# Kernel optimization log

Measured on AMD Instinct MI355X. Metric: run time of the kernel, lower is better.

The kernel has to match this reference:

```python
import jax, jax.numpy as jnp
import numpy as np

N = 100000      # num nodes
E = 1600000     # num edges
NFEAT = 512
NHID = 256
NCLASS = 32
K = 10
ALPHA = 0.1


def setup_inputs() -> dict:
    key = jax.random.key(0)
    ks = jax.random.split(key, 6)
    x = jax.random.normal(ks[0], (N, NFEAT), dtype=jnp.float32)
    edge_index = jax.random.randint(ks[1], (2, E), 0, N, dtype=jnp.int32)
    edge_attr = jax.random.uniform(ks[2], (E,), dtype=jnp.float32)
    # Linear params (Kaiming-ish scale)
    W_start = jax.random.normal(ks[3], (NFEAT, NHID), dtype=jnp.float32) * np.float32(1.0 / np.sqrt(NFEAT))
    b_start = jnp.zeros((NHID,), jnp.float32)
    W_end = jax.random.normal(ks[4], (NHID, NCLASS), dtype=jnp.float32) * np.float32(1.0 / np.sqrt(NHID))
    b_end = jnp.zeros((NCLASS,), jnp.float32)
    # GPR 'PPR' init coefficients: temp[k] = alpha*(1-alpha)^k, temp[K] = (1-alpha)^K
    temp = (ALPHA * (1.0 - ALPHA) ** np.arange(K + 1)).astype(np.float32)
    temp[-1] = np.float32((1.0 - ALPHA) ** K)
    temp = jnp.asarray(temp)
    return {"x": x, "edge_attr": edge_attr, "W_start": W_start, "b_start": b_start,
            "W_end": W_end, "b_end": b_end, "temp": temp, "edge_index": edge_index}


def gcn_norm(edge_index, edge_weight, num_nodes):
    # add self loops with weight 1 (PyG default fill_value=1)
    loop = jnp.arange(num_nodes, dtype=edge_index.dtype)
    ei = jnp.concatenate([edge_index, jnp.stack([loop, loop])], axis=1)   # [2, E+N]
    ew = jnp.concatenate([edge_weight, jnp.ones((num_nodes,), edge_weight.dtype)])
    row, col = ei[0], ei[1]
    deg = jax.ops.segment_sum(ew, col, num_segments=num_nodes)            # [N]
    dis = jnp.where(deg > 0, jax.lax.rsqrt(jnp.where(deg > 0, deg, 1.0)), 0.0)
    norm = dis[row] * ew * dis[col]                                       # [E+N]
    return ei, norm


def reference(x, edge_attr, W_start, b_start, W_end, b_end, temp, edge_index):
    # MLP front-end (eval mode: dropout is identity)
    h = jax.nn.relu(x @ W_start + b_start)        # [N, NHID]
    h = jax.nn.relu(h @ W_end + b_end)            # [N, NCLASS]
    ei, norm = gcn_norm(edge_index, edge_attr, N)
    row, col = ei[0], ei[1]
    hidden = h * temp[0]
    xk = h
    for k in range(K):
        # SpMM: gather messages norm * x[row], scatter-add at col
        xk = jax.ops.segment_sum(norm[:, None] * xk[row], col, num_segments=N)
        hidden = hidden + temp[k + 1] * xk
    return hidden
```

## Files before the change

kernel.cpp:

```cpp
#include <hip/hip_runtime.h>

typedef __attribute__((ext_vector_type(8))) short short8;
typedef __attribute__((ext_vector_type(4))) float f32x4;
typedef unsigned long long u64;

constexpr int NN = 100000;
constexpr int EE = 1600000;
constexpr int NF = 512;
constexpr int NH = 256;
constexpr int NC = 32;
constexpr int KP = 10;
constexpr int PKN = EE + 8 * NN;

__device__ __forceinline__ unsigned short f2bf(float f) {
  unsigned int u = __float_as_uint(f);
  u += 0x7FFFu + ((u >> 16) & 1u);
  return (unsigned short)(u >> 16);
}
__device__ __forceinline__ float bf2f(unsigned short s) {
  return __uint_as_float(((unsigned int)s) << 16);
}
__device__ __forceinline__ int padc(int c) { return (c + 7) & ~7; }

__device__ __forceinline__ short8 cvt8(float4 a0, float4 a1) {
  union { unsigned int u[4]; short8 s; } r;
  asm("v_cvt_pk_bf16_f32 %0, %1, %2" : "=v"(r.u[0]) : "v"(a0.x), "v"(a0.y));
  asm("v_cvt_pk_bf16_f32 %0, %1, %2" : "=v"(r.u[1]) : "v"(a0.z), "v"(a0.w));
  asm("v_cvt_pk_bf16_f32 %0, %1, %2" : "=v"(r.u[2]) : "v"(a1.x), "v"(a1.y));
  asm("v_cvt_pk_bf16_f32 %0, %1, %2" : "=v"(r.u[3]) : "v"(a1.z), "v"(a1.w));
  return r.s;
}

__device__ __forceinline__ void block_sync_lds() {
  asm volatile("s_waitcnt lgkmcnt(0)" ::: "memory");
  __builtin_amdgcn_s_barrier();
}

__global__ void convwb_kernel(const float* __restrict__ Ws, const float* __restrict__ We,
                              unsigned short* __restrict__ Wt, unsigned short* __restrict__ Web) {
  if (blockIdx.x < 32) {
    __shared__ float tile[64][65];
    const int k0 = (blockIdx.x >> 2) * 64;
    const int c0 = (blockIdx.x & 3) * 64;
    const int t = threadIdx.x;
    const int g = t >> 6, l = t & 63;
#pragma unroll
    for (int j = 0; j < 16; j++) {
      const int row = g * 16 + j;
      tile[row][l] = Ws[(size_t)(k0 + row) * NH + c0 + l];
    }
    __syncthreads();
    const int col = t >> 2, ks = (t & 3) * 16;
    union { unsigned short us[16]; short8 s8[2]; } st;
#pragma unroll
    for (int i = 0; i < 16; i++) st.us[i] = f2bf(tile[ks + i][col]);
    unsigned short* dst = Wt + (size_t)(c0 + col) * NF + k0 + ks;
    *reinterpret_cast<short8*>(dst) = st.s8[0];
    *reinterpret_cast<short8*>(dst + 8) = st.s8[1];
  } else {
    const int t = threadIdx.x;
    const int col = t & 31, kb = (t >> 5) * 32;
#pragma unroll
    for (int i = 0; i < 32; i++)
      Web[(size_t)col * 256 + kb + i] = f2bf(We[(size_t)(kb + i) * NC + col]);
  }
}

__global__ __launch_bounds__(256, 3) void gemm1_kernel(
    const float* __restrict__ X, const unsigned short* __restrict__ Wt,
    const float* __restrict__ bias, const unsigned short* __restrict__ Web,
    const float* __restrict__ be, const float* __restrict__ temp,
    unsigned short* __restrict__ x0b, float* __restrict__ out) {
  constexpr int PAD = 36;
  __shared__ __align__(16) unsigned short Asm[2][64 * PAD];
  __shared__ __align__(16) unsigned short Bsm[2][256 * PAD];
  const int tid = threadIdx.x;
  const int lane = tid & 63;
  const int w = tid >> 6;
  const int l15 = lane & 15, kq = lane >> 4;
  const int m0 = blockIdx.x * 64;

  const int arl = tid >> 2, aq = tid & 3;
  int ar = m0 + arl; if (ar >= NN) ar = NN - 1;
  const float* aptr = X + (size_t)ar * NF + aq * 8;
  const int awr = arl * PAD + aq * 8;
  const unsigned short* bptr = Wt + (size_t)tid * NF;
  const int bwr = tid * PAD;

  f32x4 acc[4][4];
#pragma unroll
  for (int m = 0; m < 4; m++)
#pragma unroll
    for (int n = 0; n < 4; n++) acc[m][n] = (f32x4)0.0f;

  float4 ra[3][2]; short8 rb[3][4];

#define LOADR(ks, j) do { \
    ra[j][0] = *reinterpret_cast<const float4*>(aptr + (ks) * 32); \
    ra[j][1] = *reinterpret_cast<const float4*>(aptr + (ks) * 32 + 4); \
    rb[j][0] = *reinterpret_cast<const short8*>(bptr + (ks) * 32); \
    rb[j][1] = *reinterpret_cast<const short8*>(bptr + (ks) * 32 + 8); \
    rb[j][2] = *reinterpret_cast<const short8*>(bptr + (ks) * 32 + 16); \
    rb[j][3] = *reinterpret_cast<const short8*>(bptr + (ks) * 32 + 24); \
  } while (0)

#define STAGE(b, j) do { \
    *reinterpret_cast<short8*>(&Asm[b][awr]) = cvt8(ra[j][0], ra[j][1]); \
    *reinterpret_cast<short8*>(&Bsm[b][bwr]) = rb[j][0]; \
    *reinterpret_cast<short8*>(&Bsm[b][bwr + 8]) = rb[j][1]; \
    *reinterpret_cast<short8*>(&Bsm[b][bwr + 16]) = rb[j][2]; \
    *reinterpret_cast<short8*>(&Bsm[b][bwr + 24]) = rb[j][3]; \
  } while (0)

#define COMPUTE(b) do { \
    short8 af[4], bfr[4]; \
    _Pragma("unroll") \
    for (int mi = 0; mi < 4; mi++) \
      af[mi] = *reinterpret_cast<const short8*>(&Asm[b][(mi * 16 + l15) * PAD + kq * 8]); \
    _Pragma("unroll") \
    for (int ni = 0; ni < 4; ni++) \
      bfr[ni] = *reinterpret_cast<const short8*>(&Bsm[b][(w * 64 + ni * 16 + l15) * PAD + kq * 8]); \
    _Pragma("unroll") \
    for (int mi = 0; mi < 4; mi++) \
      _Pragma("unroll") \
      for (int ni = 0; ni < 4; ni++) \
        acc[mi][ni] = __builtin_amdgcn_mfma_f32_16x16x32_bf16(af[mi], bfr[ni], acc[mi][ni], 0, 0, 0); \
  } while (0)

  LOADR(0, 0);
  LOADR(1, 1);
  LOADR(2, 2);
  STAGE(0, 0);
  block_sync_lds();

#pragma unroll
  for (int p = 0; p < 16; p++) {
    if (p + 3 < 16) LOADR(p + 3, (p + 3) % 3);
    COMPUTE(p & 1);
    if (p + 1 < 16) STAGE((p + 1) & 1, (p + 1) % 3);
    block_sync_lds();
  }
#undef LOADR
#undef STAGE
#undef COMPUTE

  unsigned short* Ht = (unsigned short*)Bsm;
  f32x4 acc2[2];
  acc2[0] = (f32x4)0.0f; acc2[1] = (f32x4)0.0f;
  const unsigned short* wrow = Web + (size_t)l15 * 256 + kq * 8;
#pragma unroll
  for (int p2 = 0; p2 < 2; p2++) {
    block_sync_lds();
    if ((w >> 1) == p2) {
#pragma unroll
      for (int ni = 0; ni < 4; ni++) {
        const int colg = w * 64 + ni * 16 + l15;
        const float bsv = bias[colg];
        const int cl = colg - p2 * 128;
#pragma unroll
        for (int mi = 0; mi < 4; mi++)
#pragma unroll
          for (int i = 0; i < 4; i++) {
            const int row = mi * 16 + kq * 4 + i;
            const float v = acc[mi][ni][i] + bsv;
            Ht[row * 136 + cl] = f2bf(v > 0.f ? v : 0.f);
          }
      }
    }
    block_sync_lds();
    const unsigned short* hr = Ht + (size_t)(w * 16 + l15) * 136 + kq * 8;
#pragma unroll
    for (int ks = 0; ks < 4; ks++) {
      short8 a  = *reinterpret_cast<const short8*>(hr + ks * 32);
      short8 b0 = *reinterpret_cast<const short8*>(wrow + p2 * 128 + ks * 32);
      short8 b1 = *reinterpret_cast<const short8*>(wrow + 16 * 256 + p2 * 128 + ks * 32);
      acc2[0] = __builtin_amdgcn_mfma_f32_16x16x32_bf16(a, b0, acc2[0], 0, 0, 0);
      acc2[1] = __builtin_amdgcn_mfma_f32_16x16x32_bf16(a, b1, acc2[1], 0, 0, 0);
    }
  }
  const float t0 = temp[0];
#pragma unroll
  for (int nt = 0; nt < 2; nt++) {
    const int col = nt * 16 + l15;
    const float bv = be[col];
#pragma unroll
    for (int i = 0; i < 4; i++) {
      const int row = m0 + w * 16 + kq * 4 + i;
      if (row < NN) {
        float v = acc2[nt][i] + bv;
        v = v > 0.f ? v : 0.f;
        x0b[(size_t)row * NC + col] = f2bf(v);
        out[(size_t)row * NC + col] = t0 * v;
      }
    }
  }
}

__global__ void node_init_kernel(u64* dc, u64* pk) {
  int i = blockIdx.x * 256 + threadIdx.x;
  if (i < NN) dc[i] = (1ULL << 44) | (1ULL << 32);
  for (int j = i; j < PKN; j += 391 * 256) pk[j] = 0;
}

__global__ void edge_deg_kernel(const int* __restrict__ ei, const float* __restrict__ ew,
                                u64* dc) {
  int e = blockIdx.x * 256 + threadIdx.x;
  if (e < EE) {
    int col = ei[EE + e];
    u64 v = (1ULL << 44) | (u64)((double)ew[e] * 4294967296.0);
    atomicAdd(&dc[col], v);
  }
}

__global__ void dis_kernel(const u64* __restrict__ dc, float* __restrict__ dis,
                           int* __restrict__ cnt) {
  int i = blockIdx.x * 256 + threadIdx.x;
  if (i < NN) {
    u64 v = dc[i];
    cnt[i] = (int)(v >> 44);
    float deg = (float)((double)(v & 0xFFFFFFFFFFFULL) * (1.0 / 4294967296.0));
    dis[i] = rsqrtf(deg);
  }
}

__global__ void scan1_kernel(const int* __restrict__ cnt, int* bsum) {
  __shared__ int ws[4];
  const int tid = threadIdx.x;
  int base = blockIdx.x * 1024 + tid * 4;
  int s = 0;
#pragma unroll
  for (int j = 0; j < 4; j++) { int i = base + j; if (i < NN) s += padc(cnt[i]); }
  for (int off = 32; off > 0; off >>= 1) s += __shfl_down(s, off);
  if ((tid & 63) == 0) ws[tid >> 6] = s;
  __syncthreads();
  if (tid == 0) bsum[blockIdx.x] = ws[0] + ws[1] + ws[2] + ws[3];
}

__global__ void scan3_kernel(const int* __restrict__ cnt, const int* __restrict__ bsum,
                             int* offs, int* cursor) {
  __shared__ int wsum[4];
  __shared__ int bofs_s;
  const int tid = threadIdx.x;
  const int lane = tid & 63, wv = tid >> 6;
  if (tid == 0) {
    int run = 0;
    for (int i = 0; i < (int)blockIdx.x; i++) run += bsum[i];
    bofs_s = run;
    if (blockIdx.x == 0) {
      int tot = 0;
      for (int i = 0; i < 98; i++) tot += bsum[i];
      offs[NN] = tot;
    }
  }
  int base = blockIdx.x * 1024 + tid * 4;
  int v[4]; int s = 0;
#pragma unroll
  for (int j = 0; j < 4; j++) { int i = base + j; v[j] = (i < NN) ? padc(cnt[i]) : 0; s += v[j]; }
  int incl = s;
  for (int off = 1; off < 64; off <<= 1) {
    int t = __shfl_up(incl, off);
    if (lane >= off) incl += t;
  }
  if (lane == 63) wsum[wv] = incl;
  __syncthreads();
  int woff = bofs_s;
  for (int w = 0; w < wv; w++) woff += wsum[w];
  int excl = woff + incl - s;
#pragma unroll
  for (int j = 0; j < 4; j++) {
    int i = base + j;
    if (i < NN) { offs[i] = excl; cursor[i] = excl; }
    excl += v[j];
  }
}

__global__ void fill_kernel(const int* __restrict__ ei, const float* __restrict__ ew,
                            const float* __restrict__ dis, int* cursor,
                            u64* __restrict__ pk) {
  int t = blockIdx.x * 256 + threadIdx.x;
  if (t < EE) {
    int r = ei[t], c = ei[EE + t];
    int slot = atomicAdd(&cursor[c], 1);
    unsigned int wb = __float_as_uint(dis[r] * ew[t] * dis[c]);
    pk[slot] = (u64)(unsigned int)r | ((u64)wb << 32);
  } else if (t < EE + NN) {
    int i = t - EE;
    int slot = atomicAdd(&cursor[i], 1);
    float d = dis[i];
    unsigned int wb = __float_as_uint(d * d);
    pk[slot] = (u64)(unsigned int)i | ((u64)wb << 32);
  }
}

__global__ __launch_bounds__(256) void spmm_kernel(
    const int* __restrict__ offs, const u64* __restrict__ pk,
    const unsigned short* __restrict__ xin, unsigned short* __restrict__ xout) {
  const int tid = threadIdx.x;
  const int node = blockIdx.x * 32 + (tid >> 3);
  const int fq = (tid & 7) * 4;
  const int s = offs[node], e = offs[node + 1];
  float a0 = 0.f, a1 = 0.f, a2 = 0.f, a3 = 0.f;
  for (int j = s; j < e; j += 8) {
    ulonglong2 p01 = *reinterpret_cast<const ulonglong2*>(pk + j);
    ulonglong2 p23 = *reinterpret_cast<const ulonglong2*>(pk + j + 2);
    ulonglong2 p45 = *reinterpret_cast<const ulonglong2*>(pk + j + 4);
    ulonglong2 p67 = *reinterpret_cast<const ulonglong2*>(pk + j + 6);
    const u64 p[8] = {p01.x, p01.y, p23.x, p23.y, p45.x, p45.y, p67.x, p67.y};
    u64 q[8];
#pragma unroll
    for (int i = 0; i < 8; i++)
      q[i] = *reinterpret_cast<const u64*>(xin + (size_t)(unsigned int)p[i] * NC + fq);
#pragma unroll
    for (int i = 0; i < 8; i++) {
      const float w = __uint_as_float((unsigned int)(p[i] >> 32));
      a0 += w * bf2f((unsigned short)(q[i]));
      a1 += w * bf2f((unsigned short)(q[i] >> 16));
      a2 += w * bf2f((unsigned short)(q[i] >> 32));
      a3 += w * bf2f((unsigned short)(q[i] >> 48));
    }
  }
  unsigned int lo, hi;
  asm("v_cvt_pk_bf16_f32 %0, %1, %2" : "=v"(lo) : "v"(a0), "v"(a1));
  asm("v_cvt_pk_bf16_f32 %0, %1, %2" : "=v"(hi) : "v"(a2), "v"(a3));
  *reinterpret_cast<u64*>(xout + (size_t)node * NC + fq) =
      (u64)lo | ((u64)hi << 32);
}

__global__ __launch_bounds__(256) void spmm_wsum_kernel(
    const int* __restrict__ offs, const u64* __restrict__ pk,
    const unsigned short* __restrict__ xin,
    const unsigned short* __restrict__ SL,
    float* __restrict__ out, const float* __restrict__ temp) {
  const int tid = threadIdx.x;
  const int node = blockIdx.x * 32 + (tid >> 3);
  const int fq = (tid & 7) * 4;
  const int s = offs[node], e = offs[node + 1];
  float a0 = 0.f, a1 = 0.f, a2 = 0.f, a3 = 0.f;
  for (int j = s; j < e; j += 8) {
    ulonglong2 p01 = *reinterpret_cast<const ulonglong2*>(pk + j);
    ulonglong2 p23 = *reinterpret_cast<const ulonglong2*>(pk + j + 2);
    ulonglong2 p45 = *reinterpret_cast<const ulonglong2*>(pk + j + 4);
    ulonglong2 p67 = *reinterpret_cast<const ulonglong2*>(pk + j + 6);
    const u64 p[8] = {p01.x, p01.y, p23.x, p23.y, p45.x, p45.y, p67.x, p67.y};
    u64 q[8];
#pragma unroll
    for (int i = 0; i < 8; i++)
      q[i] = *reinterpret_cast<const u64*>(xin + (size_t)(unsigned int)p[i] * NC + fq);
#pragma unroll
    for (int i = 0; i < 8; i++) {
      const float w = __uint_as_float((unsigned int)(p[i] >> 32));
      a0 += w * bf2f((unsigned short)(q[i]));
      a1 += w * bf2f((unsigned short)(q[i] >> 16));
      a2 += w * bf2f((unsigned short)(q[i] >> 32));
      a3 += w * bf2f((unsigned short)(q[i] >> 48));
    }
  }
  const size_t ob = (size_t)node * NC + fq;
  float4 o = *reinterpret_cast<const float4*>(out + ob);
  const float t10 = temp[10];
  float r0 = o.x + t10 * a0, r1 = o.y + t10 * a1;
  float r2 = o.z + t10 * a2, r3 = o.w + t10 * a3;
#pragma unroll
  for (int k = 0; k < 8; k++) {
    const float tk = temp[k + 1];
    u64 q = *reinterpret_cast<const u64*>(SL + (size_t)k * NN * NC + ob);
    r0 += tk * bf2f((unsigned short)(q));
    r1 += tk * bf2f((unsigned short)(q >> 16));
    r2 += tk * bf2f((unsigned short)(q >> 32));
    r3 += tk * bf2f((unsigned short)(q >> 48));
  }
  {
    const float tk = temp[9];
    u64 q = *reinterpret_cast<const u64*>(xin + ob);
    r0 += tk * bf2f((unsigned short)(q));
    r1 += tk * bf2f((unsigned short)(q >> 16));
    r2 += tk * bf2f((unsigned short)(q >> 32));
    r3 += tk * bf2f((unsigned short)(q >> 48));
  }
  *reinterpret_cast<float4*>(out + ob) = make_float4(r0, r1, r2, r3);
}

extern "C" void kernel_launch(void* const* d_in, const int* in_sizes, int n_in,
                              void* d_out, int out_size, void* d_ws, size_t ws_size,
                              hipStream_t stream) {
  const float* X    = (const float*)d_in[0];
  const float* EA   = (const float*)d_in[1];
  const float* Ws   = (const float*)d_in[2];
  const float* bs   = (const float*)d_in[3];
  const float* We   = (const float*)d_in[4];
  const float* be   = (const float*)d_in[5];
  const float* temp = (const float*)d_in[6];
  const int*   ei   = (const int*)d_in[7];
  float* out = (float*)d_out;

  size_t off = 0;
  auto alloc = [&](size_t n) { void* p = (char*)d_ws + off; off += (n + 255) & ~(size_t)255; return p; };
  unsigned short* Wt  = (unsigned short*)alloc((size_t)NF * NH * 2);
  unsigned short* Web = (unsigned short*)alloc((size_t)NH * NC * 2);
  unsigned short* SL  = (unsigned short*)alloc((size_t)NN * NH * 2);
  unsigned short* x0b = (unsigned short*)alloc((size_t)NN * NC * 2);
  unsigned short* xk8 = (unsigned short*)alloc((size_t)NN * NC * 2);
  u64*   dc   = (u64*)alloc((size_t)NN * 8);
  float* dis  = (float*)alloc((size_t)NN * 4);
  int*   cnt  = (int*)alloc((size_t)NN * 4);
  int*   offs = (int*)alloc((size_t)(NN + 1) * 4);
  int*   cursor = (int*)alloc((size_t)NN * 4);
  int*   bsum = (int*)alloc(98 * 4);
  u64*   pk   = (u64*)alloc((size_t)PKN * 8);

  convwb_kernel<<<33, 256, 0, stream>>>(Ws, We, Wt, Web);
  gemm1_kernel<<<1563, 256, 0, stream>>>(X, Wt, bs, Web, be, temp, x0b, out);

  node_init_kernel<<<391, 256, 0, stream>>>(dc, pk);
  edge_deg_kernel<<<6250, 256, 0, stream>>>(ei, EA, dc);
  dis_kernel<<<391, 256, 0, stream>>>(dc, dis, cnt);
  scan1_kernel<<<98, 256, 0, stream>>>(cnt, bsum);
  scan3_kernel<<<98, 256, 0, stream>>>(cnt, bsum, offs, cursor);
  fill_kernel<<<6641, 256, 0, stream>>>(ei, EA, dis, cursor, pk);

  auto slice = [&](int k) -> unsigned short* {
    return (k < 8) ? SL + (size_t)k * NN * NC : xk8;
  };
  const unsigned short* xin = x0b;
  for (int k = 0; k < KP - 1; k++) {
    spmm_kernel<<<3125, 256, 0, stream>>>(offs, pk, xin, slice(k));
    xin = slice(k);
  }
  spmm_wsum_kernel<<<3125, 256, 0, stream>>>(offs, pk, xk8, SL, out, temp);
}
```

Before: 534.6 us.

## Merge preprocessing launches and co-schedule degree atomics with the GEMM

Folds weight conversion and node/pk initialisation into one prep kernel. Appends the edge-degree atomic blocks to the GEMM launch so they run concurrently with GEMM tiles. Fuses the dis computation into the first scan pass. This removes several launches and intermediate passes over the node arrays, and lets the memory-bound atomics overlap compute-heavy GEMM work. The risk is that the extra blocks in the GEMM launch compete for occupancy, since they use the same launch bounds and LDS allocation.

Result: faster. 504.3 us (-5.7%).

```diff
diff --git a/kernel.cpp b/kernel.cpp
--- a/kernel.cpp
+++ b/kernel.cpp
@@ -11,6 +11,7 @@
 constexpr int NC = 32;
 constexpr int KP = 10;
 constexpr int PKN = EE + 8 * NN;
+constexpr int GB = 1563;
 
 __device__ __forceinline__ unsigned short f2bf(float f) {
   unsigned int u = __float_as_uint(f);
@@ -36,8 +37,9 @@
   __builtin_amdgcn_s_barrier();
 }
 
-__global__ void convwb_kernel(const float* __restrict__ Ws, const float* __restrict__ We,
-                              unsigned short* __restrict__ Wt, unsigned short* __restrict__ Web) {
+__global__ void prep_kernel(const float* __restrict__ Ws, const float* __restrict__ We,
+                            unsigned short* __restrict__ Wt, unsigned short* __restrict__ Web,
+                            u64* __restrict__ dc, u64* __restrict__ pk) {
   if (blockIdx.x < 32) {
     __shared__ float tile[64][65];
     const int k0 = (blockIdx.x >> 2) * 64;
@@ -57,24 +59,40 @@
     unsigned short* dst = Wt + (size_t)(c0 + col) * NF + k0 + ks;
     *reinterpret_cast<short8*>(dst) = st.s8[0];
     *reinterpret_cast<short8*>(dst + 8) = st.s8[1];
-  } else {
+  } else if (blockIdx.x == 32) {
     const int t = threadIdx.x;
     const int col = t & 31, kb = (t >> 5) * 32;
 #pragma unroll
     for (int i = 0; i < 32; i++)
       Web[(size_t)col * 256 + kb + i] = f2bf(We[(size_t)(kb + i) * NC + col]);
-  }
-}
-
-__global__ __launch_bounds__(256, 3) void gemm1_kernel(
+  } else {
+    const int i = (blockIdx.x - 33) * 256 + threadIdx.x;
+    if (i < NN) dc[i] = (1ULL << 44) | (1ULL << 32);
+    for (int j = i; j < PKN; j += 391 * 256) pk[j] = 0;
+  }
+}
+
+__global__ __launch_bounds__(256, 3) void gemm_deg_kernel(
     const float* __restrict__ X, const unsigned short* __restrict__ Wt,
     const float* __restrict__ bias, const unsigned short* __restrict__ Web,
     const float* __restrict__ be, const float* __restrict__ temp,
-    unsigned short* __restrict__ x0b, float* __restrict__ out) {
+    unsigned short* __restrict__ x0b, float* __restrict__ out,
+    const int* __restrict__ ei, const float* __restrict__ ew, u64* dc) {
   constexpr int PAD = 36;
   __shared__ __align__(16) unsigned short Asm[2][64 * PAD];
   __shared__ __align__(16) unsigned short Bsm[2][256 * PAD];
   const int tid = threadIdx.x;
+
+  if (blockIdx.x >= GB) {
+    const int e = (blockIdx.x - GB) * 256 + tid;
+    if (e < EE) {
+      const int col = ei[EE + e];
+      u64 v = (1ULL << 44) | (u64)((double)ew[e] * 4294967296.0);
+      atomicAdd(&dc[col], v);
+    }
+    return;
+  }
+
   const int lane = tid & 63;
   const int w = tid >> 6;
   const int l15 = lane & 15, kq = lane >> 4;
@@ -196,40 +214,24 @@
   }
 }
 
-__global__ void node_init_kernel(u64* dc, u64* pk) {
-  int i = blockIdx.x * 256 + threadIdx.x;
-  if (i < NN) dc[i] = (1ULL << 44) | (1ULL << 32);
-  for (int j = i; j < PKN; j += 391 * 256) pk[j] = 0;
-}
-
-__global__ void edge_deg_kernel(const int* __restrict__ ei, const float* __restrict__ ew,
-                                u64* dc) {
-  int e = blockIdx.x * 256 + threadIdx.x;
-  if (e < EE) {
-    int col = ei[EE + e];
-    u64 v = (1ULL << 44) | (u64)((double)ew[e] * 4294967296.0);
-    atomicAdd(&dc[col], v);
-  }
-}
-
-__global__ void dis_kernel(const u64* __restrict__ dc, float* __restrict__ dis,
-                           int* __restrict__ cnt) {
-  int i = blockIdx.x * 256 + threadIdx.x;
-  if (i < NN) {
-    u64 v = dc[i];
-    cnt[i] = (int)(v >> 44);
-    float deg = (float)((double)(v & 0xFFFFFFFFFFFULL) * (1.0 / 4294967296.0));
-    dis[i] = rsqrtf(deg);
-  }
-}
-
-__global__ void scan1_kernel(const int* __restrict__ cnt, int* bsum) {
+__global__ void dis_scan_kernel(const u64* __restrict__ dc, float* __restrict__ dis,
+                                int* __restrict__ cnt, int* bsum) {
   __shared__ int ws[4];
   const int tid = threadIdx.x;
   int base = blockIdx.x * 1024 + tid * 4;
   int s = 0;
 #pragma unroll
-  for (int j = 0; j < 4; j++) { int i = base + j; if (i < NN) s += padc(cnt[i]); }
+  for (int j = 0; j < 4; j++) {
+    int i = base + j;
+    if (i < NN) {
+      u64 v = dc[i];
+      int c = (int)(v >> 44);
+      cnt[i] = c;
+      float deg = (float)((double)(v & 0xFFFFFFFFFFFULL) * (1.0 / 4294967296.0));
+      dis[i] = rsqrtf(deg);
+      s += padc(c);
+    }
+  }
   for (int off = 32; off > 0; off >>= 1) s += __shfl_down(s, off);
   if ((tid & 63) == 0) ws[tid >> 6] = s;
   __syncthreads();
@@ -408,13 +410,12 @@
   int*   bsum = (int*)alloc(98 * 4);
   u64*   pk   = (u64*)alloc((size_t)PKN * 8);
 
-  convwb_kernel<<<33, 256, 0, stream>>>(Ws, We, Wt, Web);
-  gemm1_kernel<<<1563, 256, 0, stream>>>(X, Wt, bs, Web, be, temp, x0b, out);
-
-  node_init_kernel<<<391, 256, 0, stream>>>(dc, pk);
-  edge_deg_kernel<<<6250, 256, 0, stream>>>(ei, EA, dc);
-  dis_kernel<<<391, 256, 0, stream>>>(dc, dis, cnt);
-  scan1_kernel<<<98, 256, 0, stream>>>(cnt, bsum);
+  prep_kernel<<<424, 256, 0, stream>>>(Ws, We, Wt, Web, dc, pk);
+
+  gemm_deg_kernel<<<GB + 6250, 256, 0, stream>>>(X, Wt, bs, Web, be, temp,
+                                                 x0b, out, ei, EA, dc);
+
+  dis_scan_kernel<<<98, 256, 0, stream>>>(dc, dis, cnt, bsum);
   scan3_kernel<<<98, 256, 0, stream>>>(cnt, bsum, offs, cursor);
   fill_kernel<<<6641, 256, 0, stream>>>(ei, EA, dis, cursor, pk);
 
```
